# Kernel tuning notes

Measured on AMD Instinct MI355X. Metric: run time of the kernel, lower is better.

The kernel has to match this reference:

```python
import jax, jax.numpy as jnp
import numpy as np

N_NODES = 50000
N_EDGES = 800000
N_GRAPHS = 1024
IN_DIM, HID, OUT_DIM = 78, 256, 128
EPS = 1e-5


def setup_inputs() -> dict:
    key = jax.random.key(0)
    ks = jax.random.split(key, 12)
    def lin(k, fi, fo):
        s = 1.0 / np.sqrt(fi)
        return jax.random.uniform(k, (fi, fo), jnp.float32, -s, s)
    inp = {
        "x_l": jax.random.normal(ks[0], (N_NODES, IN_DIM), jnp.float32),
        "edge_index_l": jax.random.randint(ks[1], (2, N_EDGES), 0, N_NODES, jnp.int64),
        "batch_l": jnp.sort(jax.random.randint(ks[2], (N_NODES,), 0, N_GRAPHS, jnp.int64)),
        # GraphConv 1: 78 -> 256 (lin_rel has bias, lin_root no bias)
        "W1_rel": lin(ks[3], IN_DIM, HID), "b1_rel": jnp.zeros((HID,), jnp.float32), "W1_root": lin(ks[4], IN_DIM, HID),
        # GraphConv 2: 256 -> 512
        "W2_rel": lin(ks[5], HID, 2 * HID), "b2_rel": jnp.zeros((2 * HID,), jnp.float32), "W2_root": lin(ks[6], HID, 2 * HID),
        # GraphConv 3: 512 -> 512
        "W3_rel": lin(ks[7], 2 * HID, 2 * HID), "b3_rel": jnp.zeros((2 * HID,), jnp.float32), "W3_root": lin(ks[8], 2 * HID, 2 * HID),
        # fc1: Linear(512 -> 128) + LayerNorm(128); Dropout(0.01) is identity in eval
        "W_fc": lin(ks[9], 2 * HID, OUT_DIM), "b_fc": jnp.zeros((OUT_DIM,), jnp.float32),
        "ln_g": jnp.ones((OUT_DIM,), jnp.float32), "ln_b": jnp.zeros((OUT_DIM,), jnp.float32),
    }
    return inp


def _graph_conv(x, src, dst, W_rel, b_rel, W_root):
    # PyG GraphConv (aggr='add'): out = lin_rel(sum_{j->i} x_j) + lin_root(x_i)
    aggr = jax.ops.segment_sum(x[src], dst, num_segments=x.shape[0])  # [N, d_in]
    return aggr @ W_rel + b_rel + x @ W_root


def reference(x_l, edge_index_l, batch_l,
              W1_rel, b1_rel, W1_root,
              W2_rel, b2_rel, W2_root,
              W3_rel, b3_rel, W3_root,
              W_fc, b_fc, ln_g, ln_b):
    src, dst = edge_index_l[0], edge_index_l[1]
    h = jax.nn.relu(_graph_conv(x_l, src, dst, W1_rel, b1_rel, W1_root))
    h = jax.nn.relu(_graph_conv(h, src, dst, W2_rel, b2_rel, W2_root))
    h = jax.nn.relu(_graph_conv(h, src, dst, W3_rel, b3_rel, W3_root))
    # fc1: Linear -> LayerNorm -> Dropout(0.01, identity in eval) -> ReLU
    z = h @ W_fc + b_fc
    mu = jnp.mean(z, axis=-1, keepdims=True)
    var = jnp.mean(jnp.square(z - mu), axis=-1, keepdims=True)
    z = (z - mu) * jax.lax.rsqrt(var + EPS) * ln_g + ln_b
    x_atom = jax.nn.relu(z)  # [N, OUT_DIM]
    pooled = jax.ops.segment_sum(x_atom, batch_l, num_segments=N_GRAPHS)  # [G, OUT_DIM]
    return (x_atom, pooled)
```

## Files before the change

kernel.cpp:

```cpp
#include <hip/hip_runtime.h>

#define N_NODES 50000
#define N_EDGES 800000
#define N_GRAPHS 1024
#define IN_DIM 78
#define K1P 96
#define HID 256
#define OUT_DIM 128

typedef unsigned short ushort_t;
typedef __attribute__((ext_vector_type(8))) short v8s;
typedef __attribute__((ext_vector_type(4))) float v4f;
typedef __attribute__((ext_vector_type(4))) unsigned int u4;
typedef __attribute__((ext_vector_type(2))) unsigned short us2;
typedef __attribute__((ext_vector_type(4))) unsigned short us4;
typedef __attribute__((ext_vector_type(8))) unsigned short us8;

__device__ __forceinline__ ushort_t f2bf(float f) {
    unsigned u = __float_as_uint(f);
    unsigned r = (u + 0x7fffu + ((u >> 16) & 1u)) >> 16;
    return (ushort_t)r;
}
__device__ __forceinline__ float bf2f(ushort_t h) {
    return __uint_as_float((unsigned)h << 16);
}

__device__ __forceinline__ void gload16(const ushort_t* g, ushort_t* l) {
    __builtin_amdgcn_global_load_lds(
        (const __attribute__((address_space(1))) void*)g,
        (__attribute__((address_space(3))) void*)l, 16, 0, 0);
}

__device__ __forceinline__ int xcd_swizzle(int orig, int nwg) {
    int q = nwg >> 3, r = nwg & 7;
    int xcd = orig & 7, i = orig >> 3;
    return (xcd < r ? xcd * (q + 1) : r * (q + 1) + (xcd - r) * q) + i;
}

__global__ __launch_bounds__(256)
void wt_all_kernel(const float* __restrict__ W1r, const float* __restrict__ W1o,
                   const float* __restrict__ W2r, const float* __restrict__ W2o,
                   const float* __restrict__ W3r, const float* __restrict__ W3o,
                   const float* __restrict__ Wfc, ushort_t* __restrict__ out)
{
    int i = blockIdx.x * 256 + threadIdx.x;
    if (i >= 901120) return;
    const float* W; int K, N, Kp, base;
    if      (i < 24576)  { W = W1r; K = IN_DIM; N = HID;     Kp = 96;  base = 0; }
    else if (i < 49152)  { W = W1o; K = IN_DIM; N = HID;     Kp = 96;  base = 24576; }
    else if (i < 180224) { W = W2r; K = HID;    N = 2 * HID; Kp = 256; base = 49152; }
    else if (i < 311296) { W = W2o; K = HID;    N = 2 * HID; Kp = 256; base = 180224; }
    else if (i < 573440) { W = W3r; K = 2*HID;  N = 2 * HID; Kp = 512; base = 311296; }
    else if (i < 835584) { W = W3o; K = 2*HID;  N = 2 * HID; Kp = 512; base = 573440; }
    else                 { W = Wfc; K = 2*HID;  N = OUT_DIM; Kp = 512; base = 835584; }
    int j = i - base;
    int n = j / Kp, k = j - n * Kp;
    float v = (k < K) ? W[(size_t)k * N + n] : 0.0f;
    out[i] = f2bf(v);
}

__global__ __launch_bounds__(256)
void pad_cast_kernel(const float* __restrict__ in, ushort_t* __restrict__ out,
                     int rows, int Kin, int Kout)
{
    int i = blockIdx.x * 256 + threadIdx.x;
    if (i >= rows * Kout) return;
    int r = i / Kout, k = i - r * Kout;
    out[i] = f2bf(k < Kin ? in[(size_t)r * Kin + k] : 0.0f);
}

__global__ __launch_bounds__(256)
void hist_kernel(const int* __restrict__ dstI, int* __restrict__ deg, int nE)
{
    int e = blockIdx.x * 256 + threadIdx.x;
    if (e < nE) {
        int d = dstI[e];
        if ((unsigned)d < (unsigned)N_NODES) atomicAdd(&deg[d], 1);
    }
}

__global__ __launch_bounds__(1024)
void scan1_kernel(const int* __restrict__ deg, int* __restrict__ rowptr,
                  int* __restrict__ blocksum, int n)
{
    __shared__ int s[1024];
    int b = (int)blockIdx.x, t = (int)threadIdx.x;
    int i = b * 1024 + t;
    int v = (i < n) ? deg[i] : 0;
    s[t] = v;
    __syncthreads();
    for (int off = 1; off < 1024; off <<= 1) {
        int a = (t >= off) ? s[t - off] : 0;
        __syncthreads();
        s[t] += a;
        __syncthreads();
    }
    if (i < n) rowptr[i + 1] = s[t];
    if (t == 1023) blocksum[b] = s[1023];
    if (b == 0 && t == 0) rowptr[0] = 0;
}

__global__ __launch_bounds__(64)
void scan2_kernel(int* __restrict__ blocksum, int nb)
{
    int t = (int)threadIdx.x;
    int v = (t < nb) ? blocksum[t] : 0;
    #pragma unroll
    for (int off = 1; off < 64; off <<= 1) {
        int a = __shfl_up(v, off, 64);
        if (t >= off) v += a;
    }
    if (t < nb) blocksum[t] = v;
}

__global__ __launch_bounds__(256)
void scan3_kernel(const int* __restrict__ blocksum, int* __restrict__ rowptr,
                  int* __restrict__ cursor, int n)
{
    int j = blockIdx.x * 256 + threadIdx.x;
    if (j > n) return;
    int v;
    if (j == 0) v = 0;
    else {
        int b = (j - 1) >> 10;
        v = rowptr[j] + (b >= 1 ? blocksum[b - 1] : 0);
    }
    rowptr[j] = v;
    if (j < n) cursor[j] = v;
}

__global__ __launch_bounds__(256)
void fill_kernel(const int* __restrict__ srcI, const int* __restrict__ dstI,
                 int* __restrict__ cursor, int* __restrict__ csr_src, int nE)
{
    int e = blockIdx.x * 256 + threadIdx.x;
    if (e < nE) {
        int d = dstI[e];
        int s = srcI[e];
        if ((unsigned)d < (unsigned)N_NODES && (unsigned)s < (unsigned)N_NODES) {
            int pos = atomicAdd(&cursor[d], 1);
            csr_src[pos] = s;
        }
    }
}

template<int VPT> struct VecT;
template<> struct VecT<2> { using T = us2; };
template<> struct VecT<4> { using T = us4; };
template<> struct VecT<8> { using T = us8; };

template<int VPT>
__global__ __launch_bounds__(256)
void csr_agg_wave_kernel(const ushort_t* __restrict__ feat,
                         const int* __restrict__ rowptr,
                         const int* __restrict__ csr_src,
                         ushort_t* __restrict__ out, int Ds)
{
    using T = typename VecT<VPT>::T;
    const int wv   = (int)threadIdx.x >> 6;
    const int node = (int)blockIdx.x * 4 + wv;
    if (node >= N_NODES) return;
    const int lane = (int)threadIdx.x & 63;
    const int off0 = lane * VPT;
    const bool act = off0 < Ds;
    const int off  = act ? off0 : (Ds - VPT);

    const int e0 = rowptr[node], e1 = rowptr[node + 1];
    float acc[VPT];
    #pragma unroll
    for (int i = 0; i < VPT; ++i) acc[i] = 0.0f;

    int e = e0;
    for (; e + 8 <= e1; e += 8) {
        T r[8];
        #pragma unroll
        for (int u = 0; u < 8; ++u) {
            int s = csr_src[e + u];
            r[u] = *(const T*)(feat + (size_t)s * Ds + off);
        }
        #pragma unroll
        for (int u = 0; u < 8; ++u)
            #pragma unroll
            for (int i = 0; i < VPT; ++i) acc[i] += bf2f(r[u][i]);
    }
    for (; e + 4 <= e1; e += 4) {
        T r[4];
        #pragma unroll
        for (int u = 0; u < 4; ++u) {
            int s = csr_src[e + u];
            r[u] = *(const T*)(feat + (size_t)s * Ds + off);
        }
        #pragma unroll
        for (int u = 0; u < 4; ++u)
            #pragma unroll
            for (int i = 0; i < VPT; ++i) acc[i] += bf2f(r[u][i]);
    }
    for (; e < e1; ++e) {
        int s = csr_src[e];
        T r = *(const T*)(feat + (size_t)s * Ds + off);
        #pragma unroll
        for (int i = 0; i < VPT; ++i) acc[i] += bf2f(r[i]);
    }

    if (act) {
        T o;
        #pragma unroll
        for (int i = 0; i < VPT; ++i) o[i] = f2bf(acc[i]);
        *(T*)(out + (size_t)node * Ds + off0) = o;
    }
}

__global__ __launch_bounds__(256, 4)
void mfma_gemm_kernel(const ushort_t* __restrict__ A1,
                      const ushort_t* __restrict__ A2,
                      const ushort_t* __restrict__ W1t,
                      const ushort_t* __restrict__ W2t,
                      const float* __restrict__ bias,
                      ushort_t* __restrict__ outp,
                      int M, int K, int Fo, int relu)
{
    __shared__ __align__(16) ushort_t smem[17408];
    const int tid = (int)threadIdx.x;
    const int l   = tid & 63;
    const int w   = tid >> 6;
    const int q   = l >> 4;
    const int r15 = l & 15;
    const int wm  = w >> 1, wn = w & 1;

    const int wg = xcd_swizzle((int)blockIdx.x, (int)gridDim.x);
    const int nx = Fo >> 7;
    const int bx = wg % nx;
    const int by = wg / nx;
    const int bm = by * 128;
    const int bn = bx * 128;

    const int s1 = K >> 5;
    const int nsteps = A2 ? (2 * s1) : s1;

    int aOff[2], bOff[2];
    #pragma unroll
    for (int ii = 0; ii < 2; ++ii) {
        int ar = bm + (w * 2 + ii) * 16 + r15;
        if (ar >= M) ar = M - 1;
        aOff[ii] = ar * K;
        int bc = bn + (w * 2 + ii) * 16 + r15;
        bOff[ii] = bc * K;
    }
    const int kq = q * 8;

    auto stage = [&](int step, int buf) {
        const ushort_t* A  = (step >= s1) ? A2  : A1;
        const ushort_t* Bt = (step >= s1) ? W2t : W1t;
        const int k0 = (((step >= s1) ? (step - s1) : step) << 5) + kq;
        ushort_t* db = smem + buf * 8192;
        #pragma unroll
        for (int ii = 0; ii < 2; ++ii)
            gload16(A + aOff[ii] + k0, db + (size_t)(w * 2 + ii) * 512);
        #pragma unroll
        for (int ii = 0; ii < 2; ++ii)
            gload16(Bt + bOff[ii] + k0, db + (size_t)(8 + w * 2 + ii) * 512);
    };

    v4f acc[4][4];
    #pragma unroll
    for (int mt = 0; mt < 4; ++mt)
        #pragma unroll
        for (int nt = 0; nt < 4; ++nt)
            acc[mt][nt] = (v4f){0.0f, 0.0f, 0.0f, 0.0f};

    stage(0, 0);
    for (int step = 0; step < nsteps; ++step) {
        const int cur = step & 1;
        __syncthreads();
        if (step + 1 < nsteps) stage(step + 1, cur ^ 1);
        const ushort_t* db = smem + cur * 8192;
        v8s af[4], bf[4];
        #pragma unroll
        for (int mt = 0; mt < 4; ++mt)
            af[mt] = *(const v8s*)(db + (size_t)(wm * 4 + mt) * 512 + l * 8);
        #pragma unroll
        for (int nt = 0; nt < 4; ++nt)
            bf[nt] = *(const v8s*)(db + (size_t)(8 + wn * 4 + nt) * 512 + l * 8);
        #pragma unroll
        for (int mt = 0; mt < 4; ++mt)
            #pragma unroll
            for (int nt = 0; nt < 4; ++nt)
                acc[mt][nt] = __builtin_amdgcn_mfma_f32_16x16x32_bf16(
                    af[mt], bf[nt], acc[mt][nt], 0, 0, 0);
    }

    __syncthreads();
    #pragma unroll
    for (int nt = 0; nt < 4; ++nt) {
        int col = wn * 64 + nt * 16 + r15;
        float bb = bias[bn + col];
        #pragma unroll
        for (int mt = 0; mt < 4; ++mt) {
            int row0 = wm * 64 + mt * 16 + q * 4;
            #pragma unroll
            for (int p = 0; p < 4; ++p) {
                float v = acc[mt][nt][p] + bb;
                if (relu) v = fmaxf(v, 0.0f);
                smem[(size_t)(row0 + p) * 136 + col] = f2bf(v);
            }
        }
    }
    __syncthreads();
    #pragma unroll
    for (int pass = 0; pass < 8; ++pass) {
        int row = pass * 16 + (tid >> 4);
        int gr  = bm + row;
        if (gr < M) {
            u4 v = *(const u4*)(smem + (size_t)row * 136 + (tid & 15) * 8);
            *(u4*)(outp + (size_t)gr * Fo + bn + (tid & 15) * 8) = v;
        }
    }
}

__global__ __launch_bounds__(256, 3)
void mfma_fc_ln_kernel(const ushort_t* __restrict__ A,
                       const ushort_t* __restrict__ Wt,
                       const float* __restrict__ bias,
                       const float* __restrict__ gamma,
                       const float* __restrict__ beta,
                       const int* __restrict__ batch,
                       float* __restrict__ x_atom,
                       float* __restrict__ pooled,
                       int M, int K)
{
    __shared__ __align__(16) char smem_raw[34816];
    ushort_t* smem = (ushort_t*)smem_raw;
    float*    sf   = (float*)smem_raw;
    const int tid = (int)threadIdx.x;
    const int l   = tid & 63;
    const int w   = tid >> 6;
    const int q   = l >> 4;
    const int r15 = l & 15;
    const int wm  = w >> 1, wn = w & 1;
    const int bm  = (int)blockIdx.x * 128;
    const int nsteps = K >> 5;

    int aOff[2], bOff[2];
    #pragma unroll
    for (int ii = 0; ii < 2; ++ii) {
        int ar = bm + (w * 2 + ii) * 16 + r15;
        if (ar >= M) ar = M - 1;
        aOff[ii] = ar * K;
        bOff[ii] = ((w * 2 + ii) * 16 + r15) * K;
    }
    const int kq = q * 8;

    auto stage = [&](int step, int buf) {
        const int k0 = (step << 5) + kq;
        ushort_t* db = smem + buf * 8192;
        #pragma unroll
        for (int ii = 0; ii < 2; ++ii)
            gload16(A + aOff[ii] + k0, db + (size_t)(w * 2 + ii) * 512);
        #pragma unroll
        for (int ii = 0; ii < 2; ++ii)
            gload16(Wt + bOff[ii] + k0, db + (size_t)(8 + w * 2 + ii) * 512);
    };

    v4f acc[4][4];
    #pragma unroll
    for (int mt = 0; mt < 4; ++mt)
        #pragma unroll
        for (int nt = 0; nt < 4; ++nt)
            acc[mt][nt] = (v4f){0.0f, 0.0f, 0.0f, 0.0f};

    stage(0, 0);
    for (int step = 0; step < nsteps; ++step) {
        const int cur = step & 1;
        __syncthreads();
        if (step + 1 < nsteps) stage(step + 1, cur ^ 1);
        const ushort_t* db = smem + cur * 8192;
        v8s af[4], bf[4];
        #pragma unroll
        for (int mt = 0; mt < 4; ++mt)
            af[mt] = *(const v8s*)(db + (size_t)(wm * 4 + mt) * 512 + l * 8);
        #pragma unroll
        for (int nt = 0; nt < 4; ++nt)
            bf[nt] = *(const v8s*)(db + (size_t)(8 + wn * 4 + nt) * 512 + l * 8);
        #pragma unroll
        for (int mt = 0; mt < 4; ++mt)
            #pragma unroll
            for (int nt = 0; nt < 4; ++nt)
                acc[mt][nt] = __builtin_amdgcn_mfma_f32_16x16x32_bf16(
                    af[mt], bf[nt], acc[mt][nt], 0, 0, 0);
    }

    const int lrow = tid >> 2;
    const int c0   = (tid & 3) * 32;
    float pacc = 0.0f;
    int   pcur = -1;
    #pragma unroll
    for (int half = 0; half < 2; ++half) {
        __syncthreads();
        if (wm == half) {
            #pragma unroll
            for (int nt = 0; nt < 4; ++nt) {
                int col = wn * 64 + nt * 16 + r15;
                float bb = bias[col];
                #pragma unroll
                for (int mt = 0; mt < 4; ++mt) {
                    int row0 = mt * 16 + q * 4;
                    #pragma unroll
                    for (int p = 0; p < 4; ++p)
                        sf[(size_t)(row0 + p) * 132 + col] = acc[mt][nt][p] + bb;
                }
            }
        }
        __syncthreads();
        int gr = bm + half * 64 + lrow;
        float* rowp = sf + (size_t)lrow * 132 + c0;
        float s = 0.0f;
        #pragma unroll
        for (int j = 0; j < 32; j += 4) {
            v4f t = *(const v4f*)(rowp + j);
            s += t[0] + t[1] + t[2] + t[3];
        }
        s += __shfl_xor(s, 1, 64);
        s += __shfl_xor(s, 2, 64);
        float mean = s * (1.0f / 128.0f);
        float s2 = 0.0f;
        #pragma unroll
        for (int j = 0; j < 32; j += 4) {
            v4f t = *(const v4f*)(rowp + j);
            #pragma unroll
            for (int k = 0; k < 4; ++k) { float d = t[k] - mean; s2 += d * d; }
        }
        s2 += __shfl_xor(s2, 1, 64);
        s2 += __shfl_xor(s2, 2, 64);
        float rstd = rsqrtf(s2 * (1.0f / 128.0f) + 1e-5f);
        bool rok = gr < M;
        #pragma unroll
        for (int j = 0; j < 32; j += 4) {
            v4f t  = *(const v4f*)(rowp + j);
            v4f g  = *(const v4f*)(gamma + c0 + j);
            v4f bt = *(const v4f*)(beta + c0 + j);
            v4f y;
            #pragma unroll
            for (int k = 0; k < 4; ++k)
                y[k] = fmaxf((t[k] - mean) * rstd * g[k] + bt[k], 0.0f);
            if (rok) *(v4f*)(x_atom + (size_t)gr * 128 + c0 + j) = y;
            *(v4f*)(rowp + j) = y;
        }
        __syncthreads();
        if (tid < 128) {
            for (int r = 0; r < 64; ++r) {
                int grr = bm + half * 64 + r;
                if (grr >= M) break;
                int b = batch[grr];
                if (b != pcur) {
                    if (pcur >= 0 && pacc != 0.0f)
                        atomicAdd(pooled + (size_t)pcur * 128 + tid, pacc);
                    pcur = b; pacc = 0.0f;
                }
                pacc += sf[(size_t)r * 132 + tid];
            }
        }
    }
    if (tid < 128 && pcur >= 0)
        atomicAdd(pooled + (size_t)pcur * 128 + tid, pacc);
}

extern "C" void kernel_launch(void* const* d_in, const int* in_sizes, int n_in,
                              void* d_out, int out_size, void* d_ws, size_t ws_size,
                              hipStream_t stream)
{
    const float* x     = (const float*)d_in[0];
    const int*   ei    = (const int*)d_in[1];
    const int*   batch = (const int*)d_in[2];
    const float* W1r   = (const float*)d_in[3];
    const float* b1    = (const float*)d_in[4];
    const float* W1o   = (const float*)d_in[5];
    const float* W2r   = (const float*)d_in[6];
    const float* b2    = (const float*)d_in[7];
    const float* W2o   = (const float*)d_in[8];
    const float* W3r   = (const float*)d_in[9];
    const float* b3    = (const float*)d_in[10];
    const float* W3o   = (const float*)d_in[11];
    const float* Wfc   = (const float*)d_in[12];
    const float* bfc   = (const float*)d_in[13];
    const float* lng   = (const float*)d_in[14];
    const float* lnb   = (const float*)d_in[15];

    const size_t WS_NEED = 204800000;
    if (ws_size < WS_NEED) {
        hipMemsetAsync(d_out, 0, (size_t)out_size * sizeof(float), stream);
        return;
    }

    char* ws = (char*)d_ws;
    ushort_t* xb   = (ushort_t*)(ws + 0);
    ushort_t* h1   = (ushort_t*)(ws + 9600000);
    ushort_t* aggr = (ushort_t*)(ws + 35200000);
    ushort_t* h2   = (ushort_t*)(ws + 86400000);
    ushort_t* h3   = (ushort_t*)(ws + 137600000);
    int* deg    = (int*)(ws + 188800000);
    int* rowptr = (int*)(ws + 189000000);
    int* cursor = (int*)(ws + 189200128);
    int* csrsrc = (int*)(ws + 189400128);
    int* blksum = (int*)(ws + 192600128);
    ushort_t* wt = (ushort_t*)(ws + 192600512);
    ushort_t* w1r_t = wt;
    ushort_t* w1o_t = wt + 24576;
    ushort_t* w2r_t = wt + 49152;
    ushort_t* w2o_t = wt + 180224;
    ushort_t* w3r_t = wt + 311296;
    ushort_t* w3o_t = wt + 573440;
    ushort_t* wfc_t = wt + 835584;

    float* x_atom = (float*)d_out;
    float* pooled = x_atom + (size_t)N_NODES * OUT_DIM;

    const int* src = ei;
    const int* dst = ei + N_EDGES;

    wt_all_kernel<<<(901120 + 255) / 256, 256, 0, stream>>>(W1r, W1o, W2r, W2o,
                                                            W3r, W3o, Wfc, wt);
    pad_cast_kernel<<<((N_NODES * K1P) + 255) / 256, 256, 0, stream>>>(x, xb, N_NODES, IN_DIM, K1P);

    hipMemsetAsync(deg, 0, N_NODES * sizeof(int), stream);
    hist_kernel<<<(N_EDGES + 255) / 256, 256, 0, stream>>>(dst, deg, N_EDGES);
    {
        int nb = (N_NODES + 1023) / 1024;
        scan1_kernel<<<nb, 1024, 0, stream>>>(deg, rowptr, blksum, N_NODES);
        scan2_kernel<<<1, 64, 0, stream>>>(blksum, nb);
        scan3_kernel<<<(N_NODES + 1 + 255) / 256, 256, 0, stream>>>(blksum, rowptr, cursor, N_NODES);
    }
    fill_kernel<<<(N_EDGES + 255) / 256, 256, 0, stream>>>(src, dst, cursor, csrsrc, N_EDGES);

    const int GY = (N_NODES + 127) / 128;
    const int AGG_BLKS = (N_NODES + 3) / 4;

    csr_agg_wave_kernel<2><<<AGG_BLKS, 256, 0, stream>>>(xb, rowptr, csrsrc, aggr, K1P);
    mfma_gemm_kernel<<<(HID / 128) * GY, 256, 0, stream>>>(aggr, xb, w1r_t, w1o_t, b1, h1,
                                                           N_NODES, K1P, HID, 1);
    csr_agg_wave_kernel<4><<<AGG_BLKS, 256, 0, stream>>>(h1, rowptr, csrsrc, aggr, HID);
    mfma_gemm_kernel<<<((2 * HID) / 128) * GY, 256, 0, stream>>>(aggr, h1, w2r_t, w2o_t, b2, h2,
                                                                 N_NODES, HID, 2 * HID, 1);
    csr_agg_wave_kernel<8><<<AGG_BLKS, 256, 0, stream>>>(h2, rowptr, csrsrc, aggr, 2 * HID);
    mfma_gemm_kernel<<<((2 * HID) / 128) * GY, 256, 0, stream>>>(aggr, h2, w3r_t, w3o_t, b3, h3,
                                                                 N_NODES, 2 * HID, 2 * HID, 1);
    hipMemsetAsync(pooled, 0, (size_t)N_GRAPHS * OUT_DIM * sizeof(float), stream);
    mfma_fc_ln_kernel<<<GY, 256, 0, stream>>>(h3, wfc_t, bfc, lng, lnb, batch,
                                              x_atom, pooled, N_NODES, 2 * HID);
}
```

Before: 635.4 us.

## Load MFMA fragments directly from global into registers, dropping LDS staging

Both MFMA GEMM kernels stop staging A/B tiles through LDS with global_load_lds and instead load each wave's fragments straight from global memory into registers, double-buffered across two k-steps. This removes the per-step __syncthreads and LDS round trips. In exchange, A and B tiles are re-read from global/L2 by multiple waves (no intra-block reuse), register pressure rises, and occupancy drops (launch bounds 4 to 3). Each lane's 16-byte row-strided loads may also coalesce less well.

```diff
diff --git a/kernel.cpp b/kernel.cpp
--- a/kernel.cpp
+++ b/kernel.cpp
@@ -23,12 +23,6 @@
 }
 __device__ __forceinline__ float bf2f(ushort_t h) {
     return __uint_as_float((unsigned)h << 16);
-}
-
-__device__ __forceinline__ void gload16(const ushort_t* g, ushort_t* l) {
-    __builtin_amdgcn_global_load_lds(
-        (const __attribute__((address_space(1))) void*)g,
-        (__attribute__((address_space(3))) void*)l, 16, 0, 0);
 }
 
 __device__ __forceinline__ int xcd_swizzle(int orig, int nwg) {
@@ -210,7 +204,7 @@
     }
 }
 
-__global__ __launch_bounds__(256, 4)
+__global__ __launch_bounds__(256, 3)
 void mfma_gemm_kernel(const ushort_t* __restrict__ A1,
                       const ushort_t* __restrict__ A2,
                       const ushort_t* __restrict__ W1t,
@@ -237,59 +231,55 @@
     const int s1 = K >> 5;
     const int nsteps = A2 ? (2 * s1) : s1;
 
-    int aOff[2], bOff[2];
-    #pragma unroll
-    for (int ii = 0; ii < 2; ++ii) {
-        int ar = bm + (w * 2 + ii) * 16 + r15;
-        if (ar >= M) ar = M - 1;
-        aOff[ii] = ar * K;
-        int bc = bn + (w * 2 + ii) * 16 + r15;
-        bOff[ii] = bc * K;
-    }
-    const int kq = q * 8;
-
-    auto stage = [&](int step, int buf) {
+    int aOffD[4], bOffD[4];
+    #pragma unroll
+    for (int mt = 0; mt < 4; ++mt) {
+        int r = bm + (wm * 4 + mt) * 16 + r15;
+        if (r >= M) r = M - 1;
+        aOffD[mt] = r * K + q * 8;
+    }
+    #pragma unroll
+    for (int nt = 0; nt < 4; ++nt) {
+        int c = bn + (wn * 4 + nt) * 16 + r15;
+        bOffD[nt] = c * K + q * 8;
+    }
+
+    v4f acc[4][4];
+    #pragma unroll
+    for (int mt = 0; mt < 4; ++mt)
+        #pragma unroll
+        for (int nt = 0; nt < 4; ++nt)
+            acc[mt][nt] = (v4f){0.0f, 0.0f, 0.0f, 0.0f};
+
+    v8s a0[4], b0[4], a1[4], b1[4];
+    auto loadf = [&](int step, v8s* fa, v8s* fb) {
         const ushort_t* A  = (step >= s1) ? A2  : A1;
         const ushort_t* Bt = (step >= s1) ? W2t : W1t;
-        const int k0 = (((step >= s1) ? (step - s1) : step) << 5) + kq;
-        ushort_t* db = smem + buf * 8192;
-        #pragma unroll
-        for (int ii = 0; ii < 2; ++ii)
-            gload16(A + aOff[ii] + k0, db + (size_t)(w * 2 + ii) * 512);
-        #pragma unroll
-        for (int ii = 0; ii < 2; ++ii)
-            gload16(Bt + bOff[ii] + k0, db + (size_t)(8 + w * 2 + ii) * 512);
+        const int k0 = ((step >= s1) ? (step - s1) : step) << 5;
+        #pragma unroll
+        for (int mt = 0; mt < 4; ++mt)
+            fa[mt] = *(const v8s*)(A + aOffD[mt] + k0);
+        #pragma unroll
+        for (int nt = 0; nt < 4; ++nt)
+            fb[nt] = *(const v8s*)(Bt + bOffD[nt] + k0);
     };
-
-    v4f acc[4][4];
-    #pragma unroll
-    for (int mt = 0; mt < 4; ++mt)
-        #pragma unroll
-        for (int nt = 0; nt < 4; ++nt)
-            acc[mt][nt] = (v4f){0.0f, 0.0f, 0.0f, 0.0f};
-
-    stage(0, 0);
-    for (int step = 0; step < nsteps; ++step) {
-        const int cur = step & 1;
-        __syncthreads();
-        if (step + 1 < nsteps) stage(step + 1, cur ^ 1);
-        const ushort_t* db = smem + cur * 8192;
-        v8s af[4], bf[4];
-        #pragma unroll
-        for (int mt = 0; mt < 4; ++mt)
-            af[mt] = *(const v8s*)(db + (size_t)(wm * 4 + mt) * 512 + l * 8);
-        #pragma unroll
-        for (int nt = 0; nt < 4; ++nt)
-            bf[nt] = *(const v8s*)(db + (size_t)(8 + wn * 4 + nt) * 512 + l * 8);
+    auto mma = [&](v8s* fa, v8s* fb) {
         #pragma unroll
         for (int mt = 0; mt < 4; ++mt)
             #pragma unroll
             for (int nt = 0; nt < 4; ++nt)
                 acc[mt][nt] = __builtin_amdgcn_mfma_f32_16x16x32_bf16(
-                    af[mt], bf[nt], acc[mt][nt], 0, 0, 0);
-    }
-
-    __syncthreads();
+                    fa[mt], fb[nt], acc[mt][nt], 0, 0, 0);
+    };
+
+    loadf(0, a0, b0);
+    for (int step = 0; step < nsteps; step += 2) {
+        loadf(step + 1, a1, b1);
+        mma(a0, b0);
+        if (step + 2 < nsteps) loadf(step + 2, a0, b0);
+        mma(a1, b1);
+    }
+
     #pragma unroll
     for (int nt = 0; nt < 4; ++nt) {
         int col = wn * 64 + nt * 16 + r15;
@@ -328,9 +318,7 @@
                        float* __restrict__ pooled,
                        int M, int K)
 {
-    __shared__ __align__(16) char smem_raw[34816];
-    ushort_t* smem = (ushort_t*)smem_raw;
-    float*    sf   = (float*)smem_raw;
+    __shared__ __align__(16) float sf[64 * 132];
     const int tid = (int)threadIdx.x;
     const int l   = tid & 63;
     const int w   = tid >> 6;
@@ -340,26 +328,18 @@
     const int bm  = (int)blockIdx.x * 128;
     const int nsteps = K >> 5;
 
-    int aOff[2], bOff[2];
-    #pragma unroll
-    for (int ii = 0; ii < 2; ++ii) {
-        int ar = bm + (w * 2 + ii) * 16 + r15;
-        if (ar >= M) ar = M - 1;
-        aOff[ii] = ar * K;
-        bOff[ii] = ((w * 2 + ii) * 16 + r15) * K;
-    }
-    const int kq = q * 8;
-
-    auto stage = [&](int step, int buf) {
-        const int k0 = (step << 5) + kq;
-        ushort_t* db = smem + buf * 8192;
-        #pragma unroll
-        for (int ii = 0; ii < 2; ++ii)
-            gload16(A + aOff[ii] + k0, db + (size_t)(w * 2 + ii) * 512);
-        #pragma unroll
-        for (int ii = 0; ii < 2; ++ii)
-            gload16(Wt + bOff[ii] + k0, db + (size_t)(8 + w * 2 + ii) * 512);
-    };
+    int aOffD[4], bOffD[4];
+    #pragma unroll
+    for (int mt = 0; mt < 4; ++mt) {
+        int r = bm + (wm * 4 + mt) * 16 + r15;
+        if (r >= M) r = M - 1;
+        aOffD[mt] = r * K + q * 8;
+    }
+    #pragma unroll
+    for (int nt = 0; nt < 4; ++nt) {
+        int c = wn * 64 + nt * 16 + r15;
+        bOffD[nt] = c * K + q * 8;
+    }
 
     v4f acc[4][4];
     #pragma unroll
@@ -368,25 +348,31 @@
         for (int nt = 0; nt < 4; ++nt)
             acc[mt][nt] = (v4f){0.0f, 0.0f, 0.0f, 0.0f};
 
-    stage(0, 0);
-    for (int step = 0; step < nsteps; ++step) {
-        const int cur = step & 1;
-        __syncthreads();
-        if (step + 1 < nsteps) stage(step + 1, cur ^ 1);
-        const ushort_t* db = smem + cur * 8192;
-        v8s af[4], bf[4];
+    v8s a0[4], b0[4], a1[4], b1[4];
+    auto loadf = [&](int step, v8s* fa, v8s* fb) {
+        const int k0 = step << 5;
         #pragma unroll
         for (int mt = 0; mt < 4; ++mt)
-            af[mt] = *(const v8s*)(db + (size_t)(wm * 4 + mt) * 512 + l * 8);
+            fa[mt] = *(const v8s*)(A + aOffD[mt] + k0);
         #pragma unroll
         for (int nt = 0; nt < 4; ++nt)
-            bf[nt] = *(const v8s*)(db + (size_t)(8 + wn * 4 + nt) * 512 + l * 8);
+            fb[nt] = *(const v8s*)(Wt + bOffD[nt] + k0);
+    };
+    auto mma = [&](v8s* fa, v8s* fb) {
         #pragma unroll
         for (int mt = 0; mt < 4; ++mt)
             #pragma unroll
             for (int nt = 0; nt < 4; ++nt)
                 acc[mt][nt] = __builtin_amdgcn_mfma_f32_16x16x32_bf16(
-                    af[mt], bf[nt], acc[mt][nt], 0, 0, 0);
+                    fa[mt], fb[nt], acc[mt][nt], 0, 0, 0);
+    };
+
+    loadf(0, a0, b0);
+    for (int step = 0; step < nsteps; step += 2) {
+        loadf(step + 1, a1, b1);
+        mma(a0, b0);
+        if (step + 2 < nsteps) loadf(step + 2, a0, b0);
+        mma(a1, b1);
     }
 
     const int lrow = tid >> 2;
```

Result: slower. 781.8 us (+23.0%).
